# Performance work log

Hardware: AMD Instinct MI355X
Metric: run time of the kernel (lower is better)

Reference implementation:

```python
import jax, jax.numpy as jnp
import numpy as np

B, N, D, LAT, EC = 1024, 256, 64, 128, 32


def setup_inputs() -> dict:
    key = jax.random.key(0)
    ks = jax.random.split(key, 8)
    s = lambda d: 1.0 / np.sqrt(d)
    return {
        "local_data": jax.random.normal(ks[0], (B, D), jnp.float32),
        "neighbor_data": jax.random.normal(ks[1], (B, N, D), jnp.float32),
        "Wc": jax.random.normal(ks[2], (D, EC), jnp.float32) * s(D),
        "bc": jnp.zeros((EC,), jnp.float32),
        "Wf": jax.random.normal(ks[3], (D, LAT), jnp.float32) * s(D),
        "bf": jnp.zeros((LAT,), jnp.float32),
        "Wa": jax.random.normal(ks[4], (3 * EC, LAT), jnp.float32) * s(3 * EC),
        "ba": jnp.zeros((LAT,), jnp.float32),
        "Wl": jax.random.normal(ks[5], (LAT, LAT), jnp.float32) * s(LAT),
        "bl": jnp.zeros((LAT,), jnp.float32),
    }


def reference(local_data, neighbor_data, Wc, bc, Wf, bf, Wa, ba, Wl, bl):
    # per-neighbor feature encoder: [B,N,LAT]
    enc_feature = jax.nn.relu(jnp.einsum("bnd,dk->bnk", neighbor_data, Wf) + bf)
    # per-neighbor communication encoder: [B,N,EC]
    enc_comm = jax.nn.relu(jnp.einsum("bnd,dk->bnk", neighbor_data, Wc) + bc)
    # self communication embedding: [B,EC]
    enc_comm_self = jax.nn.relu(local_data @ Wc + bc)
    # broadcast self and neighbor-mean to [B,N,EC]
    self_rep = jnp.broadcast_to(enc_comm_self[:, None, :], enc_comm.shape)
    mean_rep = jnp.broadcast_to(enc_comm.mean(axis=1, keepdims=True), enc_comm.shape)
    cat = jnp.concatenate([self_rep, enc_comm, mean_rep], axis=-1)  # [B,N,3*EC]
    # attention: linear then softmax over neighbor axis (dim=-2)
    att = jax.nn.softmax(jnp.einsum("bnc,ck->bnk", cat, Wa) + ba, axis=1)  # [B,N,LAT]
    # attention-weighted sum over neighbors: [B,LAT]
    aggregated = jnp.einsum("bnk,bnk->bk", att, enc_feature)
    # later layer
    return jax.nn.relu(aggregated @ Wl + bl)
```

## Files before the change

### kernel.cpp

```cpp
#include <hip/hip_runtime.h>

#define NB    256
#define DIN   64
#define LATD  128
#define ECD   32

typedef __attribute__((ext_vector_type(8))) __bf16 bf16x8;
typedef __attribute__((ext_vector_type(4))) float f32x4;

#define XS_STRIDE 72
#define EC_STRIDE 40
#define WA_STRIDE 40

#define WS_WC 0
#define WS_WF (32 * 72)
#define WS_WA (32 * 72 + 128 * 72)
#define WSTAGE_SHORTS (128 * 72 + 128 * 40)
#define WA_OFF (128 * 72)

#define MFMA(a, b, c) __builtin_amdgcn_mfma_f32_16x16x32_bf16((a), (b), (c), 0, 0, 0)

__device__ __forceinline__ unsigned short f2bf(float f) {
    unsigned u = __builtin_bit_cast(unsigned, f);
    u += 0x7fffu + ((u >> 16) & 1u);
    return (unsigned short)(u >> 16);
}

__device__ __forceinline__ unsigned cvt2(float lo, float hi) {
    unsigned r;
    asm("v_cvt_pk_bf16_f32 %0, %1, %2" : "=v"(r) : "v"(lo), "v"(hi));
    return r;
}

#if __has_builtin(__builtin_amdgcn_exp2f)
__device__ __forceinline__ float fexp2(float x) {
    return __builtin_amdgcn_exp2f(x);
}
#else
__device__ __forceinline__ float fexp2(float x) {
    float r;
    asm("v_exp_f32 %0, %1\n\ts_nop 1" : "=v"(r) : "v"(x));
    return r;
}
#endif

__device__ __forceinline__ bf16x8 pack8(float4 a, float4 b) {
    union { unsigned u[4]; bf16x8 v; } r;
    r.u[0] = cvt2(a.x, a.y);
    r.u[1] = cvt2(a.z, a.w);
    r.u[2] = cvt2(b.x, b.y);
    r.u[3] = cvt2(b.z, b.w);
    return r.v;
}

__global__ __launch_bounds__(256) void prep_kernel(
    const float* __restrict__ Wc, const float* __restrict__ Wf,
    const float* __restrict__ Wa, unsigned short* __restrict__ ws)
{
    int t = blockIdx.x * blockDim.x + threadIdx.x;
    int stride = gridDim.x * blockDim.x;
    for (int i = t; i < 32 * 64; i += stride) {
        int n = i >> 6, k = i & 63;
        ws[WS_WC + n * XS_STRIDE + k] = f2bf(Wc[k * ECD + n]);
    }
    for (int i = t; i < 128 * 64; i += stride) {
        int n = i >> 6, k = i & 63;
        ws[WS_WF + n * XS_STRIDE + k] = f2bf(Wf[k * LATD + n]);
    }
    for (int i = t; i < 128 * 32; i += stride) {
        int n = i >> 5, k = i & 31;
        ws[WS_WA + n * WA_STRIDE + k] = f2bf(Wa[(ECD + k) * LATD + n] * 1.44269504f);
    }
}

__global__ __launch_bounds__(256, 2) void arm_main(
    const float* __restrict__ xg,
    const float* __restrict__ bcv,
    const float* __restrict__ bfv,
    const float* __restrict__ wl,
    const float* __restrict__ blv,
    const unsigned short* __restrict__ ws,
    float* __restrict__ out)
{
    __shared__ unsigned short wstage[WSTAGE_SHORTS];
    __shared__ float bfs[LATD];
    __shared__ unsigned short ecs[NB * EC_STRIDE];
    __shared__ float aggnum[2][4][LATD];
    __shared__ float aggden[2][4][LATD];
    __shared__ float aggfull[2][LATD];
    __shared__ float wlpart[2][2][LATD];

    const int b0   = blockIdx.x;
    const int b1   = blockIdx.x + 512;
    const int tid  = threadIdx.x;
    const int lane = tid & 63;
    const int w    = tid >> 6;
    const int l15  = lane & 15;
    const int q    = lane >> 4;

    uint4 wch[7];
    {
        const uint4* src = reinterpret_cast<const uint4*>(ws + WS_WF);
        #pragma unroll
        for (int i = 0; i < 7; ++i)
            wch[i] = src[tid + i * 256];
    }
    uint4 bfch;
    if (tid < 32) bfch = reinterpret_cast<const uint4*>(bfv)[tid];

    bf16x8 wfrag[2][2];
    #pragma unroll
    for (int ks = 0; ks < 2; ++ks)
        #pragma unroll
        for (int nb = 0; nb < 2; ++nb)
            wfrag[ks][nb] = *reinterpret_cast<const bf16x8*>(
                &ws[WS_WC + (nb * 16 + l15) * XS_STRIDE + ks * 32 + q * 8]);
    float bc0 = bcv[l15], bc1 = bcv[16 + l15];

    float4 st0[4][4], st1[4][4];
    {
        const float* xa = xg + (size_t)b0 * NB * DIN;
        const float* xc = xg + (size_t)b1 * NB * DIN;
        #pragma unroll
        for (int t = 0; t < 4; ++t) {
            const float* p = xa + (w * 64 + t * 16 + l15) * DIN + q * 8;
            st0[t][0] = *reinterpret_cast<const float4*>(p);
            st0[t][1] = *reinterpret_cast<const float4*>(p + 4);
            st0[t][2] = *reinterpret_cast<const float4*>(p + 32);
            st0[t][3] = *reinterpret_cast<const float4*>(p + 36);
        }
        #pragma unroll
        for (int t = 0; t < 4; ++t) {
            const float* p = xc + (w * 64 + t * 16 + l15) * DIN + q * 8;
            st1[t][0] = *reinterpret_cast<const float4*>(p);
            st1[t][1] = *reinterpret_cast<const float4*>(p + 4);
            st1[t][2] = *reinterpret_cast<const float4*>(p + 32);
            st1[t][3] = *reinterpret_cast<const float4*>(p + 36);
        }
    }

    {
        uint4* dst = reinterpret_cast<uint4*>(wstage);
        #pragma unroll
        for (int i = 0; i < 7; ++i)
            dst[tid + i * 256] = wch[i];
        if (tid < 32) reinterpret_cast<uint4*>(bfs)[tid] = bfch;
    }

    bf16x8 xfrag[2][4][2];
    #pragma unroll
    for (int t = 0; t < 4; ++t) {
        xfrag[0][t][0] = pack8(st0[t][0], st0[t][1]);
        xfrag[0][t][1] = pack8(st0[t][2], st0[t][3]);
    }
    #pragma unroll
    for (int t = 0; t < 4; ++t) {
        xfrag[1][t][0] = pack8(st1[t][0], st1[t][1]);
        xfrag[1][t][1] = pack8(st1[t][2], st1[t][3]);
    }

    bf16x8 ecfrag[2][4];
    #pragma unroll
    for (int e = 0; e < 2; ++e) {
        #pragma unroll
        for (int t = 0; t < 4; ++t) {
            int rowA = w * 64 + t * 16;
            f32x4 a0 = {bc0, bc0, bc0, bc0};
            f32x4 a1 = {bc1, bc1, bc1, bc1};
            #pragma unroll
            for (int ks = 0; ks < 2; ++ks) {
                a0 = MFMA(xfrag[e][t][ks], wfrag[ks][0], a0);
                a1 = MFMA(xfrag[e][t][ks], wfrag[ks][1], a1);
            }
            #pragma unroll
            for (int r = 0; r < 4; ++r) {
                int row = rowA + q * 4 + r;
                unsigned pk = cvt2(fmaxf(a0[r], 0.f), fmaxf(a1[r], 0.f));
                ecs[row * EC_STRIDE + l15]      = (unsigned short)pk;
                ecs[row * EC_STRIDE + 16 + l15] = (unsigned short)(pk >> 16);
            }
        }
        #pragma unroll
        for (int t = 0; t < 4; ++t)
            ecfrag[e][t] = *reinterpret_cast<const bf16x8*>(
                &ecs[(w * 64 + t * 16 + l15) * EC_STRIDE + q * 8]);
    }

    __syncthreads();

    for (int g = 0; g < 8; ++g) {
        const int r0 = g * 16 + l15;
        bf16x8 wf0 = *reinterpret_cast<const bf16x8*>(&wstage[r0 * XS_STRIDE + q * 8]);
        bf16x8 wf1 = *reinterpret_cast<const bf16x8*>(&wstage[r0 * XS_STRIDE + 32 + q * 8]);
        bf16x8 wag = *reinterpret_cast<const bf16x8*>(&wstage[WA_OFF + r0 * WA_STRIDE + q * 8]);
        float  bfl = bfs[r0];

        float num0 = 0.f, den0 = 0.f, num1 = 0.f, den1 = 0.f;
        #pragma unroll
        for (int t = 0; t < 4; ++t) {
            f32x4 za = {bfl, bfl, bfl, bfl};
            za = MFMA(xfrag[0][t][0], wf0, za);
            f32x4 efa = MFMA(xfrag[0][t][1], wf1, za);
            f32x4 zz0 = {0.f, 0.f, 0.f, 0.f};
            f32x4 lga = MFMA(ecfrag[0][t], wag, zz0);
            f32x4 zb = {bfl, bfl, bfl, bfl};
            zb = MFMA(xfrag[1][t][0], wf0, zb);
            f32x4 efb = MFMA(xfrag[1][t][1], wf1, zb);
            f32x4 zz1 = {0.f, 0.f, 0.f, 0.f};
            f32x4 lgb = MFMA(ecfrag[1][t], wag, zz1);
            #pragma unroll
            for (int r = 0; r < 4; ++r) {
                float ea = fmaxf(efa[r], 0.f);
                float pa = fexp2(lga[r]);
                num0 = fmaf(pa, ea, num0);
                den0 += pa;
                float eb = fmaxf(efb[r], 0.f);
                float pb = fexp2(lgb[r]);
                num1 = fmaf(pb, eb, num1);
                den1 += pb;
            }
        }
        num0 += __shfl_xor(num0, 16, 64); num0 += __shfl_xor(num0, 32, 64);
        den0 += __shfl_xor(den0, 16, 64); den0 += __shfl_xor(den0, 32, 64);
        num1 += __shfl_xor(num1, 16, 64); num1 += __shfl_xor(num1, 32, 64);
        den1 += __shfl_xor(den1, 16, 64); den1 += __shfl_xor(den1, 32, 64);
        if (lane < 16) {
            aggnum[0][w][g * 16 + lane] = num0;
            aggden[0][w][g * 16 + lane] = den0;
            aggnum[1][w][g * 16 + lane] = num1;
            aggden[1][w][g * 16 + lane] = den1;
        }
    }
    __syncthreads();

    {
        int e = tid >> 7, c = tid & 127;
        float num = aggnum[e][0][c] + aggnum[e][1][c] + aggnum[e][2][c] + aggnum[e][3][c];
        float den = aggden[e][0][c] + aggden[e][1][c] + aggden[e][2][c] + aggden[e][3][c];
        aggfull[e][c] = num / den;
    }
    __syncthreads();

    {
        int c = tid & 127, h = tid >> 7;
        float acc0 = 0.f, acc1 = 0.f;
        #pragma unroll 16
        for (int k = h * 64; k < h * 64 + 64; ++k) {
            float wv = wl[k * LATD + c];
            acc0 = fmaf(aggfull[0][k], wv, acc0);
            acc1 = fmaf(aggfull[1][k], wv, acc1);
        }
        wlpart[h][0][c] = acc0;
        wlpart[h][1][c] = acc1;
    }
    __syncthreads();
    {
        int e = tid >> 7, c = tid & 127;
        out[(size_t)(e ? b1 : b0) * LATD + c] =
            fmaxf(wlpart[0][e][c] + wlpart[1][e][c] + blv[c], 0.f);
    }
}

extern "C" void kernel_launch(void* const* d_in, const int* in_sizes, int n_in,
                              void* d_out, int out_size, void* d_ws, size_t ws_size,
                              hipStream_t stream)
{
    const float* xg  = (const float*)d_in[1];
    const float* wc  = (const float*)d_in[2];
    const float* bc_ = (const float*)d_in[3];
    const float* wf  = (const float*)d_in[4];
    const float* bf_ = (const float*)d_in[5];
    const float* wa  = (const float*)d_in[6];
    const float* wl  = (const float*)d_in[8];
    const float* bl_ = (const float*)d_in[9];
    unsigned short* wsp = (unsigned short*)d_ws;
    float* out = (float*)d_out;

    prep_kernel<<<8, 256, 0, stream>>>(wc, wf, wa, wsp);
    arm_main<<<512, 256, 0, stream>>>(xg, bc_, bf_, wl, bl_, wsp, out);
}
```

Baseline: 123.5 us.

## Process four batch elements per block and overlap input loads with encoding

Each block now handles four batch elements instead of two, launching 256 blocks of 256 threads, one per CU. Weight staging and the per-g weight fragment loads are shared across four elements. Next-element input loads are interleaved with bf16 packing and comm encoding, and shared memory is aliased in a single arena to fit the larger footprint. The cost is more registers (launch bounds lowered to one block per CU) and lower wave occupancy, which may reduce latency hiding.

```diff
diff --git a/kernel.cpp b/kernel.cpp
--- a/kernel.cpp
+++ b/kernel.cpp
@@ -73,7 +73,7 @@
     }
 }
 
-__global__ __launch_bounds__(256, 2) void arm_main(
+__global__ __launch_bounds__(256, 1) void arm_main(
     const float* __restrict__ xg,
     const float* __restrict__ bcv,
     const float* __restrict__ bfv,
@@ -82,16 +82,15 @@
     const unsigned short* __restrict__ ws,
     float* __restrict__ out)
 {
-    __shared__ unsigned short wstage[WSTAGE_SHORTS];
-    __shared__ float bfs[LATD];
-    __shared__ unsigned short ecs[NB * EC_STRIDE];
-    __shared__ float aggnum[2][4][LATD];
-    __shared__ float aggden[2][4][LATD];
-    __shared__ float aggfull[2][LATD];
-    __shared__ float wlpart[2][2][LATD];
-
-    const int b0   = blockIdx.x;
-    const int b1   = blockIdx.x + 512;
+    __shared__ __align__(16) unsigned char arena[51712];
+    unsigned short* wstage = reinterpret_cast<unsigned short*>(arena);
+    unsigned short* ecs    = reinterpret_cast<unsigned short*>(arena + 28672);
+    float* aggnum  = reinterpret_cast<float*>(arena + 28672);
+    float* aggden  = reinterpret_cast<float*>(arena + 28672 + 8192);
+    float* aggfull = reinterpret_cast<float*>(arena + 28672 + 16384);
+    float* wlpartm = reinterpret_cast<float*>(arena + 28672 + 18432);
+    float* bfs     = reinterpret_cast<float*>(arena + 28672 + 22528);
+
     const int tid  = threadIdx.x;
     const int lane = tid & 63;
     const int w    = tid >> 6;
@@ -117,27 +116,58 @@
                 &ws[WS_WC + (nb * 16 + l15) * XS_STRIDE + ks * 32 + q * 8]);
     float bc0 = bcv[l15], bc1 = bcv[16 + l15];
 
-    float4 st0[4][4], st1[4][4];
-    {
-        const float* xa = xg + (size_t)b0 * NB * DIN;
-        const float* xc = xg + (size_t)b1 * NB * DIN;
-        #pragma unroll
-        for (int t = 0; t < 4; ++t) {
-            const float* p = xa + (w * 64 + t * 16 + l15) * DIN + q * 8;
-            st0[t][0] = *reinterpret_cast<const float4*>(p);
-            st0[t][1] = *reinterpret_cast<const float4*>(p + 4);
-            st0[t][2] = *reinterpret_cast<const float4*>(p + 32);
-            st0[t][3] = *reinterpret_cast<const float4*>(p + 36);
-        }
-        #pragma unroll
-        for (int t = 0; t < 4; ++t) {
-            const float* p = xc + (w * 64 + t * 16 + l15) * DIN + q * 8;
-            st1[t][0] = *reinterpret_cast<const float4*>(p);
-            st1[t][1] = *reinterpret_cast<const float4*>(p + 4);
-            st1[t][2] = *reinterpret_cast<const float4*>(p + 32);
-            st1[t][3] = *reinterpret_cast<const float4*>(p + 36);
-        }
-    }
+    const int xrow = (w * 64 + l15) * DIN + q * 8;
+    float4 stA[4][4], stB[4][4];
+    bf16x8 xfrag[4][4][2];
+    bf16x8 ecfrag[4][4];
+
+#define XLOAD(dst, bidx)                                                      \
+    {                                                                         \
+        const float* xb = xg + (size_t)(bidx) * NB * DIN + xrow;              \
+        _Pragma("unroll")                                                     \
+        for (int t = 0; t < 4; ++t) {                                         \
+            const float* p = xb + t * 16 * DIN;                               \
+            dst[t][0] = *reinterpret_cast<const float4*>(p);                  \
+            dst[t][1] = *reinterpret_cast<const float4*>(p + 4);              \
+            dst[t][2] = *reinterpret_cast<const float4*>(p + 32);             \
+            dst[t][3] = *reinterpret_cast<const float4*>(p + 36);             \
+        }                                                                     \
+    }
+
+#define PACK_ENC(e, src)                                                      \
+    {                                                                         \
+        _Pragma("unroll")                                                     \
+        for (int t = 0; t < 4; ++t) {                                         \
+            xfrag[e][t][0] = pack8(src[t][0], src[t][1]);                     \
+            xfrag[e][t][1] = pack8(src[t][2], src[t][3]);                     \
+        }                                                                     \
+        _Pragma("unroll")                                                     \
+        for (int t = 0; t < 4; ++t) {                                         \
+            int rowA = w * 64 + t * 16;                                       \
+            f32x4 a0 = {bc0, bc0, bc0, bc0};            \
+            f32x4 a1 = {bc1, bc1, bc1, bc1};                                  \
+            _Pragma("unroll")                                                 \
+            for (int ks = 0; ks < 2; ++ks) {                                  \
+                a0 = MFMA(xfrag[e][t][ks], wfrag[ks][0], a0);                 \
+                a1 = MFMA(xfrag[e][t][ks], wfrag[ks][1], a1);                 \
+            }                                                                 \
+            _Pragma("unroll")                                                 \
+            for (int r = 0; r < 4; ++r) {                                     \
+                int row = rowA + q * 4 + r;      \
+                unsigned pk = cvt2(fmaxf(a0[r], 0.f), fmaxf(a1[r], 0.f));     \
+                ecs[row * EC_STRIDE + l15]      = (unsigned short)pk;         \
+                ecs[row * EC_STRIDE + 16 + l15] = (unsigned short)(pk >> 16); \
+            }                                                                 \
+        }                                                                     \
+        _Pragma("unroll")                                                     \
+        for (int t = 0; t < 4; ++t)                                           \
+            ecfrag[e][t] = *reinterpret_cast<const bf16x8*>(                  \
+                &ecs[(w * 64 + t * 16 + l15) * EC_STRIDE + q * 8]);           \
+    }
+
+    const int b0 = blockIdx.x;
+    XLOAD(stA, b0);
+    XLOAD(stB, b0 + 256);
 
     {
         uint4* dst = reinterpret_cast<uint4*>(wstage);
@@ -147,44 +177,12 @@
         if (tid < 32) reinterpret_cast<uint4*>(bfs)[tid] = bfch;
     }
 
-    bf16x8 xfrag[2][4][2];
-    #pragma unroll
-    for (int t = 0; t < 4; ++t) {
-        xfrag[0][t][0] = pack8(st0[t][0], st0[t][1]);
-        xfrag[0][t][1] = pack8(st0[t][2], st0[t][3]);
-    }
-    #pragma unroll
-    for (int t = 0; t < 4; ++t) {
-        xfrag[1][t][0] = pack8(st1[t][0], st1[t][1]);
-        xfrag[1][t][1] = pack8(st1[t][2], st1[t][3]);
-    }
-
-    bf16x8 ecfrag[2][4];
-    #pragma unroll
-    for (int e = 0; e < 2; ++e) {
-        #pragma unroll
-        for (int t = 0; t < 4; ++t) {
-            int rowA = w * 64 + t * 16;
-            f32x4 a0 = {bc0, bc0, bc0, bc0};
-            f32x4 a1 = {bc1, bc1, bc1, bc1};
-            #pragma unroll
-            for (int ks = 0; ks < 2; ++ks) {
-                a0 = MFMA(xfrag[e][t][ks], wfrag[ks][0], a0);
-                a1 = MFMA(xfrag[e][t][ks], wfrag[ks][1], a1);
-            }
-            #pragma unroll
-            for (int r = 0; r < 4; ++r) {
-                int row = rowA + q * 4 + r;
-                unsigned pk = cvt2(fmaxf(a0[r], 0.f), fmaxf(a1[r], 0.f));
-                ecs[row * EC_STRIDE + l15]      = (unsigned short)pk;
-                ecs[row * EC_STRIDE + 16 + l15] = (unsigned short)(pk >> 16);
-            }
-        }
-        #pragma unroll
-        for (int t = 0; t < 4; ++t)
-            ecfrag[e][t] = *reinterpret_cast<const bf16x8*>(
-                &ecs[(w * 64 + t * 16 + l15) * EC_STRIDE + q * 8]);
-    }
+    PACK_ENC(0, stA);
+    XLOAD(stA, b0 + 512);
+    PACK_ENC(1, stB);
+    XLOAD(stB, b0 + 768);
+    PACK_ENC(2, stA);
+    PACK_ENC(3, stB);
 
     __syncthreads();
 
@@ -195,70 +193,84 @@
         bf16x8 wag = *reinterpret_cast<const bf16x8*>(&wstage[WA_OFF + r0 * WA_STRIDE + q * 8]);
         float  bfl = bfs[r0];
 
-        float num0 = 0.f, den0 = 0.f, num1 = 0.f, den1 = 0.f;
+        float num[4] = {0.f, 0.f, 0.f, 0.f};
+        float den[4] = {0.f, 0.f, 0.f, 0.f};
         #pragma unroll
         for (int t = 0; t < 4; ++t) {
-            f32x4 za = {bfl, bfl, bfl, bfl};
-            za = MFMA(xfrag[0][t][0], wf0, za);
-            f32x4 efa = MFMA(xfrag[0][t][1], wf1, za);
-            f32x4 zz0 = {0.f, 0.f, 0.f, 0.f};
-            f32x4 lga = MFMA(ecfrag[0][t], wag, zz0);
-            f32x4 zb = {bfl, bfl, bfl, bfl};
-            zb = MFMA(xfrag[1][t][0], wf0, zb);
-            f32x4 efb = MFMA(xfrag[1][t][1], wf1, zb);
-            f32x4 zz1 = {0.f, 0.f, 0.f, 0.f};
-            f32x4 lgb = MFMA(ecfrag[1][t], wag, zz1);
             #pragma unroll
-            for (int r = 0; r < 4; ++r) {
-                float ea = fmaxf(efa[r], 0.f);
-                float pa = fexp2(lga[r]);
-                num0 = fmaf(pa, ea, num0);
-                den0 += pa;
-                float eb = fmaxf(efb[r], 0.f);
-                float pb = fexp2(lgb[r]);
-                num1 = fmaf(pb, eb, num1);
-                den1 += pb;
+            for (int e = 0; e < 4; ++e) {
+                f32x4 z = {bfl, bfl, bfl, bfl};
+                z = MFMA(xfrag[e][t][0], wf0, z);
+                f32x4 ef = MFMA(xfrag[e][t][1], wf1, z);
+                f32x4 zz = {0.f, 0.f, 0.f, 0.f};
+                f32x4 lg = MFMA(ecfrag[e][t], wag, zz);
+                #pragma unroll
+                for (int r = 0; r < 4; ++r) {
+                    float ev = fmaxf(ef[r], 0.f);
+                    float p  = fexp2(lg[r]);
+                    num[e] = fmaf(p, ev, num[e]);
+                    den[e] += p;
+                }
             }
         }
-        num0 += __shfl_xor(num0, 16, 64); num0 += __shfl_xor(num0, 32, 64);
-        den0 += __shfl_xor(den0, 16, 64); den0 += __shfl_xor(den0, 32, 64);
-        num1 += __shfl_xor(num1, 16, 64); num1 += __shfl_xor(num1, 32, 64);
-        den1 += __shfl_xor(den1, 16, 64); den1 += __shfl_xor(den1, 32, 64);
+        #pragma unroll
+        for (int e = 0; e < 4; ++e) {
+            num[e] += __shfl_xor(num[e], 16, 64);
+            num[e] += __shfl_xor(num[e], 32, 64);
+            den[e] += __shfl_xor(den[e], 16, 64);
+            den[e] += __shfl_xor(den[e], 32, 64);
+        }
         if (lane < 16) {
-            aggnum[0][w][g * 16 + lane] = num0;
-            aggden[0][w][g * 16 + lane] = den0;
-            aggnum[1][w][g * 16 + lane] = num1;
-            aggden[1][w][g * 16 + lane] = den1;
-        }
-    }
-    __syncthreads();
-
-    {
-        int e = tid >> 7, c = tid & 127;
-        float num = aggnum[e][0][c] + aggnum[e][1][c] + aggnum[e][2][c] + aggnum[e][3][c];
-        float den = aggden[e][0][c] + aggden[e][1][c] + aggden[e][2][c] + aggden[e][3][c];
-        aggfull[e][c] = num / den;
+            #pragma unroll
+            for (int e = 0; e < 4; ++e) {
+                aggnum[(e * 4 + w) * LATD + g * 16 + lane] = num[e];
+                aggden[(e * 4 + w) * LATD + g * 16 + lane] = den[e];
+            }
+        }
+    }
+    __syncthreads();
+
+    {
+        int c = tid & 127, eh = tid >> 7;
+        #pragma unroll
+        for (int e0 = 0; e0 < 2; ++e0) {
+            int e = eh + e0 * 2;
+            float num = aggnum[(e * 4 + 0) * LATD + c] + aggnum[(e * 4 + 1) * LATD + c]
+                      + aggnum[(e * 4 + 2) * LATD + c] + aggnum[(e * 4 + 3) * LATD + c];
+            float den = aggden[(e * 4 + 0) * LATD + c] + aggden[(e * 4 + 1) * LATD + c]
+                      + aggden[(e * 4 + 2) * LATD + c] + aggden[(e * 4 + 3) * LATD + c];
+            aggfull[e * LATD + c] = num / den;
+        }
     }
     __syncthreads();
 
     {
         int c = tid & 127, h = tid >> 7;
-        float acc0 = 0.f, acc1 = 0.f;
+        float acc[4] = {0.f, 0.f, 0.f, 0.f};
         #pragma unroll 16
         for (int k = h * 64; k < h * 64 + 64; ++k) {
             float wv = wl[k * LATD + c];
-            acc0 = fmaf(aggfull[0][k], wv, acc0);
-            acc1 = fmaf(aggfull[1][k], wv, acc1);
-        }
-        wlpart[h][0][c] = acc0;
-        wlpart[h][1][c] = acc1;
-    }
-    __syncthreads();
-    {
-        int e = tid >> 7, c = tid & 127;
-        out[(size_t)(e ? b1 : b0) * LATD + c] =
-            fmaxf(wlpart[0][e][c] + wlpart[1][e][c] + blv[c], 0.f);
-    }
+            #pragma unroll
+            for (int e = 0; e < 4; ++e)
+                acc[e] = fmaf(aggfull[e * LATD + k], wv, acc[e]);
+        }
+        #pragma unroll
+        for (int e = 0; e < 4; ++e)
+            wlpartm[(h * 4 + e) * LATD + c] = acc[e];
+    }
+    __syncthreads();
+    {
+        int c = tid & 127, eh = tid >> 7;
+        #pragma unroll
+        for (int e0 = 0; e0 < 2; ++e0) {
+            int e = eh + e0 * 2;
+            out[(size_t)(b0 + e * 256) * LATD + c] =
+                fmaxf(wlpartm[(0 * 4 + e) * LATD + c] +
+                      wlpartm[(1 * 4 + e) * LATD + c] + blv[c], 0.f);
+        }
+    }
+#undef XLOAD
+#undef PACK_ENC
 }
 
 extern "C" void kernel_launch(void* const* d_in, const int* in_sizes, int n_in,
@@ -277,5 +289,5 @@
     float* out = (float*)d_out;
 
     prep_kernel<<<8, 256, 0, stream>>>(wc, wf, wa, wsp);
-    arm_main<<<512, 256, 0, stream>>>(xg, bc_, bf_, wl, bl_, wsp, out);
-}
+    arm_main<<<256, 256, 0, stream>>>(xg, bc_, bf_, wl, bl_, wsp, out);
+}
```

After: 130.1 us. +5.3%, slower.
